# Kernel optimization log

Measured on AMD Instinct MI355X. Metric: run time of the kernel, lower is better.

The kernel has to match this reference:

```python
import jax, jax.numpy as jnp
import numpy as np

BATCH = 262144
LATENT_DIM = 128
N_CLUSTERS = 10


def setup_inputs() -> dict:
    key = jax.random.key(0)
    kz, kc = jax.random.split(key)
    z = jax.random.normal(kz, (BATCH, LATENT_DIM), dtype=jnp.float32)
    cluster_centers = jax.random.normal(kc, (N_CLUSTERS, LATENT_DIM), dtype=jnp.float32)
    return {"z": z, "cluster_centers": cluster_centers}


def reference(z, cluster_centers):
    # Student's-t soft assignment (alpha = 1):
    # q_ij = (1 + ||z_i - mu_j||^2)^-1, power ((alpha+1)/2) == 1
    # squared distances: [B, K]
    sq_dist = jnp.sum(jnp.square(z[:, None, :] - cluster_centers[None, :, :]), axis=2)
    q = 1.0 / (1.0 + sq_dist)
    q = q ** ((1.0 + 1.0) / 2.0)
    q = q / jnp.sum(q, axis=1, keepdims=True)  # row-normalize

    # target distribution p
    weight = q ** 2 / jnp.sum(q, axis=0)            # [B, K] / [K]
    p = weight / jnp.sum(weight, axis=1, keepdims=True)
    return (q, p)
```

## Files before the change

kernel.cpp:

```cpp
#include <hip/hip_runtime.h>
#include <stdint.h>

#define NB 262144
#define D 128
#define K 10

#define BLK_THREADS 256
#define ROWS_PER_BLK 512
#define NBLK1 (NB / ROWS_PER_BLK)
#define CHUNK 16
#define NCHUNK (D / CHUNK)

__global__ __launch_bounds__(BLK_THREADS) void qkern(
    const float* __restrict__ z, const float* __restrict__ centers,
    float* __restrict__ qout, float* __restrict__ f) {
  __shared__ float buf[2][ROWS_PER_BLK * CHUNK];
  __shared__ float c_lds[K * D];
  __shared__ float red[4][K];

  const int t = threadIdx.x;
  const int w = t >> 6;
  const int lane = t & 63;
  const int row0 = blockIdx.x * ROWS_PER_BLK;

  for (int i = t; i < K * D; i += BLK_THREADS) c_lds[i] = centers[i];
  __syncthreads();

  auto stage = [&](int cb, int c) {
    const float* zc = z + (size_t)row0 * D + c * CHUNK;
#pragma unroll
    for (int i = 0; i < 8; ++i) {
      int ubase = w * 512 + i * 64;
      int unit = ubase + lane;
      int r = unit >> 2;
      int d4 = (unit & 3) ^ ((r >> 1) & 3);
      const float* src = zc + r * D + d4 * 4;
      float* dst = &buf[cb][ubase * 4];
      __builtin_amdgcn_global_load_lds(
          (const __attribute__((address_space(1))) void*)src,
          (__attribute__((address_space(3))) void*)dst, 16, 0, 0);
    }
  };

  float acc[2][K];
#pragma unroll
  for (int r2 = 0; r2 < 2; ++r2)
#pragma unroll
    for (int j = 0; j < K; ++j) acc[r2][j] = 0.f;

  stage(0, 0);
  for (int c = 0; c < NCHUNK; ++c) {
    const int cur = c & 1;
    if (c + 1 < NCHUNK) {
      stage(cur ^ 1, c + 1);
      asm volatile("s_waitcnt vmcnt(8)" ::: "memory");
    } else {
      asm volatile("s_waitcnt vmcnt(0)" ::: "memory");
    }
    __builtin_amdgcn_s_barrier();

#pragma unroll
    for (int s = 0; s < 4; ++s) {
      float4 zf[2];
#pragma unroll
      for (int r2 = 0; r2 < 2; ++r2) {
        int r = t + r2 * 256;
        int slot = s ^ ((r >> 1) & 3);
        zf[r2] = *reinterpret_cast<const float4*>(&buf[cur][(r * 4 + slot) * 4]);
      }
#pragma unroll
      for (int j = 0; j < K; ++j) {
        float4 cf = *reinterpret_cast<const float4*>(&c_lds[j * D + c * CHUNK + s * 4]);
#pragma unroll
        for (int r2 = 0; r2 < 2; ++r2) {
          float dx = zf[r2].x - cf.x; acc[r2][j] = fmaf(dx, dx, acc[r2][j]);
          float dy = zf[r2].y - cf.y; acc[r2][j] = fmaf(dy, dy, acc[r2][j]);
          float dz = zf[r2].z - cf.z; acc[r2][j] = fmaf(dz, dz, acc[r2][j]);
          float dw = zf[r2].w - cf.w; acc[r2][j] = fmaf(dw, dw, acc[r2][j]);
        }
      }
    }
    asm volatile("s_waitcnt lgkmcnt(0)" ::: "memory");
    __builtin_amdgcn_s_barrier();
  }

  float colp[K];
#pragma unroll
  for (int j = 0; j < K; ++j) colp[j] = 0.f;

#pragma unroll
  for (int r2 = 0; r2 < 2; ++r2) {
    float qu[K];
    float srow = 0.f;
#pragma unroll
    for (int j = 0; j < K; ++j) {
      qu[j] = 1.0f / (1.0f + acc[r2][j]);
      srow += qu[j];
    }
    float inv = 1.0f / srow;
    int row = row0 + t + r2 * 256;
    float* qo = qout + (size_t)row * K;
#pragma unroll
    for (int j = 0; j < K; j += 2) {
      float a = qu[j] * inv, b = qu[j + 1] * inv;
      *reinterpret_cast<float2*>(&qo[j]) = make_float2(a, b);
      colp[j] += a;
      colp[j + 1] += b;
    }
  }

#pragma unroll
  for (int j = 0; j < K; ++j) {
#pragma unroll
    for (int off = 32; off >= 1; off >>= 1)
      colp[j] += __shfl_xor(colp[j], off);
  }
  if (lane == 0) {
#pragma unroll
    for (int j = 0; j < K; ++j) red[w][j] = colp[j];
  }
  __syncthreads();
  if (t < K) {
    float s = red[0][t] + red[1][t] + red[2][t] + red[3][t];
    atomicAdd(&f[t], s);
  }
}

__global__ __launch_bounds__(256) void pkern(
    const float* __restrict__ q, const float* __restrict__ f,
    float* __restrict__ p) {
  int row = blockIdx.x * 256 + threadIdx.x;
  const float* qr = q + (size_t)row * K;
  float wv[K];
  float s = 0.f;
#pragma unroll
  for (int j = 0; j < K; j += 2) {
    float2 qq = *reinterpret_cast<const float2*>(&qr[j]);
    wv[j] = qq.x * qq.x / f[j];
    wv[j + 1] = qq.y * qq.y / f[j + 1];
    s += wv[j] + wv[j + 1];
  }
  float inv = 1.0f / s;
  float* pr = p + (size_t)row * K;
#pragma unroll
  for (int j = 0; j < K; j += 2) {
    *reinterpret_cast<float2*>(&pr[j]) = make_float2(wv[j] * inv, wv[j + 1] * inv);
  }
}

extern "C" void kernel_launch(void* const* d_in, const int* in_sizes, int n_in,
                              void* d_out, int out_size, void* d_ws, size_t ws_size,
                              hipStream_t stream) {
  const float* z = (const float*)d_in[0];
  const float* centers = (const float*)d_in[1];
  float* out = (float*)d_out;
  float* f = (float*)d_ws;

  hipMemsetAsync(d_ws, 0, K * sizeof(float), stream);
  qkern<<<NBLK1, BLK_THREADS, 0, stream>>>(z, centers, out, f);
  pkern<<<NB / 256, 256, 0, stream>>>(out, f, out + (size_t)NB * K);
}
```

Measured before the change: 213.5 us.

## Split each row across four lanes with direct global loads and shuffle reduction

Replaces the LDS double-buffered staging of z with direct float4 global loads, assigning four threads per row, each covering interleaved 4-float slices, and combining partial distances via lane shuffles. A grid-stride loop over 2048 blocks replaces the one-block-per-512-rows layout. The intent is to drop the LDS staging, barriers and waitcnt pipelining and raise occupancy by freeing shared memory. The cost is redundant epilogue work: only one lane in four computes and stores q, and there are extra shuffles.

Result: slower. 252.4 us (+18.2%).

```diff
diff --git a/kernel.cpp b/kernel.cpp
--- a/kernel.cpp
+++ b/kernel.cpp
@@ -5,115 +5,82 @@
 #define D 128
 #define K 10
 
-#define BLK_THREADS 256
-#define ROWS_PER_BLK 512
-#define NBLK1 (NB / ROWS_PER_BLK)
-#define CHUNK 16
-#define NCHUNK (D / CHUNK)
+#define QBLOCKS 2048
+#define QTHREADS 256
+#define QITERS (NB * 4 / (QBLOCKS * QTHREADS))
 
-__global__ __launch_bounds__(BLK_THREADS) void qkern(
+__global__ __launch_bounds__(QTHREADS) void qkern(
     const float* __restrict__ z, const float* __restrict__ centers,
     float* __restrict__ qout, float* __restrict__ f) {
-  __shared__ float buf[2][ROWS_PER_BLK * CHUNK];
   __shared__ float c_lds[K * D];
   __shared__ float red[4][K];
 
   const int t = threadIdx.x;
   const int w = t >> 6;
   const int lane = t & 63;
-  const int row0 = blockIdx.x * ROWS_PER_BLK;
 
-  for (int i = t; i < K * D; i += BLK_THREADS) c_lds[i] = centers[i];
+  for (int i = t; i < K * D; i += QTHREADS) c_lds[i] = centers[i];
   __syncthreads();
-
-  auto stage = [&](int cb, int c) {
-    const float* zc = z + (size_t)row0 * D + c * CHUNK;
-#pragma unroll
-    for (int i = 0; i < 8; ++i) {
-      int ubase = w * 512 + i * 64;
-      int unit = ubase + lane;
-      int r = unit >> 2;
-      int d4 = (unit & 3) ^ ((r >> 1) & 3);
-      const float* src = zc + r * D + d4 * 4;
-      float* dst = &buf[cb][ubase * 4];
-      __builtin_amdgcn_global_load_lds(
-          (const __attribute__((address_space(1))) void*)src,
-          (__attribute__((address_space(3))) void*)dst, 16, 0, 0);
-    }
-  };
-
-  float acc[2][K];
-#pragma unroll
-  for (int r2 = 0; r2 < 2; ++r2)
-#pragma unroll
-    for (int j = 0; j < K; ++j) acc[r2][j] = 0.f;
-
-  stage(0, 0);
-  for (int c = 0; c < NCHUNK; ++c) {
-    const int cur = c & 1;
-    if (c + 1 < NCHUNK) {
-      stage(cur ^ 1, c + 1);
-      asm volatile("s_waitcnt vmcnt(8)" ::: "memory");
-    } else {
-      asm volatile("s_waitcnt vmcnt(0)" ::: "memory");
-    }
-    __builtin_amdgcn_s_barrier();
-
-#pragma unroll
-    for (int s = 0; s < 4; ++s) {
-      float4 zf[2];
-#pragma unroll
-      for (int r2 = 0; r2 < 2; ++r2) {
-        int r = t + r2 * 256;
-        int slot = s ^ ((r >> 1) & 3);
-        zf[r2] = *reinterpret_cast<const float4*>(&buf[cur][(r * 4 + slot) * 4]);
-      }
-#pragma unroll
-      for (int j = 0; j < K; ++j) {
-        float4 cf = *reinterpret_cast<const float4*>(&c_lds[j * D + c * CHUNK + s * 4]);
-#pragma unroll
-        for (int r2 = 0; r2 < 2; ++r2) {
-          float dx = zf[r2].x - cf.x; acc[r2][j] = fmaf(dx, dx, acc[r2][j]);
-          float dy = zf[r2].y - cf.y; acc[r2][j] = fmaf(dy, dy, acc[r2][j]);
-          float dz = zf[r2].z - cf.z; acc[r2][j] = fmaf(dz, dz, acc[r2][j]);
-          float dw = zf[r2].w - cf.w; acc[r2][j] = fmaf(dw, dw, acc[r2][j]);
-        }
-      }
-    }
-    asm volatile("s_waitcnt lgkmcnt(0)" ::: "memory");
-    __builtin_amdgcn_s_barrier();
-  }
 
   float colp[K];
 #pragma unroll
   for (int j = 0; j < K; ++j) colp[j] = 0.f;
 
+  for (int it = 0; it < QITERS; ++it) {
+    const int g = (blockIdx.x + it * QBLOCKS) * QTHREADS + t;
+    const int r = g >> 2;
+    const int sub = g & 3;
+
+    float acc[K];
 #pragma unroll
-  for (int r2 = 0; r2 < 2; ++r2) {
-    float qu[K];
-    float srow = 0.f;
+    for (int j = 0; j < K; ++j) acc[j] = 0.f;
+
+    const float* zr = z + (size_t)r * D + sub * 4;
+#pragma unroll
+    for (int k = 0; k < 8; ++k) {
+      float4 zv = *reinterpret_cast<const float4*>(&zr[k * 16]);
+#pragma unroll
+      for (int j = 0; j < K; ++j) {
+        float4 cv = *reinterpret_cast<const float4*>(&c_lds[j * D + k * 16 + sub * 4]);
+        float dx = zv.x - cv.x; acc[j] = fmaf(dx, dx, acc[j]);
+        float dy = zv.y - cv.y; acc[j] = fmaf(dy, dy, acc[j]);
+        float dz = zv.z - cv.z; acc[j] = fmaf(dz, dz, acc[j]);
+        float dw = zv.w - cv.w; acc[j] = fmaf(dw, dw, acc[j]);
+      }
+    }
 #pragma unroll
     for (int j = 0; j < K; ++j) {
-      qu[j] = 1.0f / (1.0f + acc[r2][j]);
-      srow += qu[j];
+      acc[j] += __shfl_xor(acc[j], 1);
+      acc[j] += __shfl_xor(acc[j], 2);
     }
-    float inv = 1.0f / srow;
-    int row = row0 + t + r2 * 256;
-    float* qo = qout + (size_t)row * K;
+
+    if (sub == 0) {
+      float qu[K];
+      float srow = 0.f;
 #pragma unroll
-    for (int j = 0; j < K; j += 2) {
-      float a = qu[j] * inv, b = qu[j + 1] * inv;
-      *reinterpret_cast<float2*>(&qo[j]) = make_float2(a, b);
-      colp[j] += a;
-      colp[j + 1] += b;
+      for (int j = 0; j < K; ++j) {
+        qu[j] = 1.0f / (1.0f + acc[j]);
+        srow += qu[j];
+      }
+      float inv = 1.0f / srow;
+#pragma unroll
+      for (int j = 0; j < K; ++j) {
+        qu[j] *= inv;
+        colp[j] += qu[j];
+      }
+      float* qo = qout + (size_t)r * K;
+      *reinterpret_cast<float4*>(&qo[0]) = make_float4(qu[0], qu[1], qu[2], qu[3]);
+      *reinterpret_cast<float4*>(&qo[4]) = make_float4(qu[4], qu[5], qu[6], qu[7]);
+      *reinterpret_cast<float2*>(&qo[8]) = make_float2(qu[8], qu[9]);
     }
   }
 
 #pragma unroll
   for (int j = 0; j < K; ++j) {
-#pragma unroll
-    for (int off = 32; off >= 1; off >>= 1)
-      colp[j] += __shfl_xor(colp[j], off);
+    colp[j] += __shfl_xor(colp[j], 4);
+    colp[j] += __shfl_xor(colp[j], 8);
+    colp[j] += __shfl_xor(colp[j], 16);
+    colp[j] += __shfl_xor(colp[j], 32);
   }
   if (lane == 0) {
 #pragma unroll
@@ -157,6 +124,6 @@
   float* f = (float*)d_ws;
 
   hipMemsetAsync(d_ws, 0, K * sizeof(float), stream);
-  qkern<<<NBLK1, BLK_THREADS, 0, stream>>>(z, centers, out, f);
+  qkern<<<QBLOCKS, QTHREADS, 0, stream>>>(z, centers, out, f);
   pkern<<<NB / 256, 256, 0, stream>>>(out, f, out + (size_t)NB * K);
 }
```
